# Optimization experiments

Measured on AMD Instinct MI355X. Metric: run time of the kernel, lower is better.

The kernel has to match this reference:

```python
import jax, jax.numpy as jnp
import numpy as np

D_X, D_Y, HIDDEN, K = 256, 32, 256, 2
T = 50
SIG_MIN, SIG_MAX = 0.002, 1.0
N = 4096
D_XY = D_X + D_Y
D_IN = D_XY + 2 * HIDDEN  # 800


def setup_inputs() -> dict:
    key = jax.random.key(0)
    ks = jax.random.split(key, 12)
    def w(k, shape, fan):
        return (jax.random.normal(k, shape, jnp.float32) / np.sqrt(fan)).astype(jnp.float32)
    return {
        "xy0": jax.random.normal(ks[0], (N, D_XY), jnp.float32) * SIG_MAX,  # randn * sigma_max * extra_noise(=1)
        "t0": jax.random.randint(ks[1], (N,), 0, K),
        "t_embed": w(ks[2], (K, HIDDEN), 1),
        "tm_w1": w(ks[3], (1, HIDDEN), 1), "tm_b1": jnp.zeros((HIDDEN,), jnp.float32),
        "tm_w2": w(ks[4], (HIDDEN, HIDDEN), HIDDEN), "tm_b2": jnp.zeros((HIDDEN,), jnp.float32),
        "tr_w1": w(ks[5], (D_IN, HIDDEN), D_IN), "tr_b1": jnp.zeros((HIDDEN,), jnp.float32),
        "tr_w2": w(ks[6], (HIDDEN, HIDDEN), HIDDEN), "tr_b2": jnp.zeros((HIDDEN,), jnp.float32),
        "sh_w": w(ks[7], (HIDDEN, D_XY), HIDDEN), "sh_b": jnp.zeros((D_XY,), jnp.float32),
        "ch_w": w(ks[8], (HIDDEN, K), HIDDEN), "ch_b": jnp.zeros((K,), jnp.float32),
    }


def _sigma(t):
    return SIG_MIN * (SIG_MAX / SIG_MIN) ** t


def reference(xy0, t0, t_embed, tm_w1, tm_b1, tm_w2, tm_b2,
              tr_w1, tr_b1, tr_w2, tr_b2, sh_w, sh_b, ch_w, ch_b):
    n = xy0.shape[0]
    silu = jax.nn.silu
    base_key = jax.random.key(42)

    def net(xy, t, tau):
        te = t_embed[t]  # (n, H) embedding lookup
        # time_mlp on scalar tau -> (H,), broadcast over batch (tau is identical per row)
        tm = silu(tau * tm_w1[0] + tm_b1) @ tm_w2 + tm_b2
        tm = jnp.broadcast_to(tm, (n, HIDDEN))
        h = jnp.concatenate([xy, te, tm], axis=-1)  # (n, D_IN)
        h = silu(silu(h @ tr_w1 + tr_b1) @ tr_w2 + tr_b2)
        return h @ sh_w + sh_b, h @ ch_w + ch_b  # score (n, D_XY), logits (n, K)

    def body(carry, t_idx):
        xy, t = carry
        tau = t_idx.astype(jnp.float32) / T
        sig_t = _sigma(tau)
        sig_prev = _sigma((t_idx - 1).astype(jnp.float32) / T)
        step = sig_t ** 2 - sig_prev ** 2  # positive reverse-SDE step size
        score, logits = net(xy, t, tau)
        k1, k2 = jax.random.split(jax.random.fold_in(base_key, t_idx))
        xy = xy + step * score + jnp.sqrt(step) * jax.random.normal(k1, xy.shape, xy.dtype)
        t = jax.random.categorical(k2, logits, axis=-1)  # multinomial(softmax(logits), 1)
        return (xy, t), None

    steps = jnp.arange(T - 1, 0, -1)  # reversed(range(1, T))
    (xy, t), _ = jax.lax.scan(body, (xy0, t0), steps)
    return xy[:, :D_X], xy[:, D_X:], t
```

## Files before the change

### kernel.cpp

```cpp
#include <hip/hip_runtime.h>
#include <math.h>


#define DXY 288
#define HID 256
#define NTHR 512
#define XYP 292
#define HP  260
#define OUT_Y_OFF 1048576
#define OUT_T_OFF 1179648
#define STEP_OFF 25600
#define WS_SWE 25728

typedef unsigned int u32;

__device__ __forceinline__ void tf2x32(u32 k0, u32 k1, u32 x0, u32 x1, u32& o0, u32& o1) {
  u32 ks2 = k0 ^ k1 ^ 0x1BD11BDAu;
#define TFR(r) { x0 += x1; x1 = (x1 << (r)) | (x1 >> (32 - (r))); x1 ^= x0; }
  x0 += k0; x1 += k1;
  TFR(13) TFR(15) TFR(26) TFR(6)
  x0 += k1;  x1 += ks2 + 1u;
  TFR(17) TFR(29) TFR(16) TFR(24)
  x0 += ks2; x1 += k0 + 2u;
  TFR(13) TFR(15) TFR(26) TFR(6)
  x0 += k0;  x1 += k1 + 3u;
  TFR(17) TFR(29) TFR(16) TFR(24)
  x0 += k1;  x1 += ks2 + 4u;
  TFR(13) TFR(15) TFR(26) TFR(6)
  x0 += ks2; x1 += k0 + 5u;
#undef TFR
  o0 = x0; o1 = x1;
}

__device__ __forceinline__ u32 pbits(u32 ka, u32 kb, u32 j) {
  u32 w0, w1;
  tf2x32(ka, kb, 0u, j, w0, w1);
  return w0 ^ w1;
}

__device__ __forceinline__ float u01f(u32 bits) {
  union { u32 i; float f; } v;
  v.i = (bits >> 9) | 0x3F800000u;
  return v.f - 1.0f;
}

__device__ __forceinline__ float erfinv32(float x) {
  float w = -log1pf(-x * x);
  float p;
  if (w < 5.0f) {
    w -= 2.5f;
    p = 2.81022636e-08f;
    p = fmaf(p, w, 3.43273939e-07f);
    p = fmaf(p, w, -3.5233877e-06f);
    p = fmaf(p, w, -4.39150654e-06f);
    p = fmaf(p, w, 0.00021858087f);
    p = fmaf(p, w, -0.00125372503f);
    p = fmaf(p, w, -0.00417768164f);
    p = fmaf(p, w, 0.246640727f);
    p = fmaf(p, w, 1.50140941f);
  } else {
    w = sqrtf(w) - 3.0f;
    p = -0.000200214257f;
    p = fmaf(p, w, 0.000100950558f);
    p = fmaf(p, w, 0.00134934322f);
    p = fmaf(p, w, -0.00367342844f);
    p = fmaf(p, w, 0.00573950773f);
    p = fmaf(p, w, -0.0076224613f);
    p = fmaf(p, w, 0.00943887047f);
    p = fmaf(p, w, 1.00167406f);
    p = fmaf(p, w, 2.83297682f);
  }
  return p * x;
}

__device__ __forceinline__ float nrmf(u32 bits) {
  float val = fmaf(u01f(bits), 2.0f, -0.99999994f);
  return 1.41421356f * erfinv32(val);
}
__device__ __forceinline__ float gumf(u32 bits) {
  float u = fmaxf(u01f(bits), 1.17549435e-38f);
  return -logf(-logf(u));
}
__device__ __forceinline__ float siluf(float x) {
  return x / (1.0f + expf(-x));
}

struct B8 { float4 a0, a1, a2, a3, b0, b1, b2, b3; };

__device__ __forceinline__ void fma8x4(float acc[4], const float4 x0, const float4 x1, const B8& B) {
  acc[0]=fmaf(x0.x,B.a0.x,acc[0]); acc[1]=fmaf(x0.x,B.a0.y,acc[1]); acc[2]=fmaf(x0.x,B.a0.z,acc[2]); acc[3]=fmaf(x0.x,B.a0.w,acc[3]);
  acc[0]=fmaf(x0.y,B.a1.x,acc[0]); acc[1]=fmaf(x0.y,B.a1.y,acc[1]); acc[2]=fmaf(x0.y,B.a1.z,acc[2]); acc[3]=fmaf(x0.y,B.a1.w,acc[3]);
  acc[0]=fmaf(x0.z,B.a2.x,acc[0]); acc[1]=fmaf(x0.z,B.a2.y,acc[1]); acc[2]=fmaf(x0.z,B.a2.z,acc[2]); acc[3]=fmaf(x0.z,B.a2.w,acc[3]);
  acc[0]=fmaf(x0.w,B.a3.x,acc[0]); acc[1]=fmaf(x0.w,B.a3.y,acc[1]); acc[2]=fmaf(x0.w,B.a3.z,acc[2]); acc[3]=fmaf(x0.w,B.a3.w,acc[3]);
  acc[0]=fmaf(x1.x,B.b0.x,acc[0]); acc[1]=fmaf(x1.x,B.b0.y,acc[1]); acc[2]=fmaf(x1.x,B.b0.z,acc[2]); acc[3]=fmaf(x1.x,B.b0.w,acc[3]);
  acc[0]=fmaf(x1.y,B.b1.x,acc[0]); acc[1]=fmaf(x1.y,B.b1.y,acc[1]); acc[2]=fmaf(x1.y,B.b1.z,acc[2]); acc[3]=fmaf(x1.y,B.b1.w,acc[3]);
  acc[0]=fmaf(x1.z,B.b2.x,acc[0]); acc[1]=fmaf(x1.z,B.b2.y,acc[1]); acc[2]=fmaf(x1.z,B.b2.z,acc[2]); acc[3]=fmaf(x1.z,B.b2.w,acc[3]);
  acc[0]=fmaf(x1.w,B.b3.x,acc[0]); acc[1]=fmaf(x1.w,B.b3.y,acc[1]); acc[2]=fmaf(x1.w,B.b3.z,acc[2]); acc[3]=fmaf(x1.w,B.b3.w,acc[3]);
}

__device__ __forceinline__ void gll16(const float* g, float* l) {
  __builtin_amdgcn_global_load_lds((const __attribute__((address_space(1))) void*)g,
                                   (__attribute__((address_space(3))) void*)l, 16, 0, 0);
}

__device__ __forceinline__ void issue_stage(int seq, float* buf, int tid,
                                            const float* w1, const float* w2,
                                            const float* sw) {
  if (seq < 17) {
    const float* src = (seq < 9) ? (w1 + seq * 8192) : (w2 + (seq - 9) * 8192);
    #pragma unroll
    for (int j = 0; j < 4; ++j) {
      int u = j * 512 + tid;
      gll16(src + u * 4, buf + u * 4);
    }
  } else {
    const int t0 = (seq - 17) * 32;
    #pragma unroll
    for (int j = 0; j < 4; ++j) {
      int u = j * 512 + tid;
      int r = u >> 6, c4 = (u & 63) << 2;
      gll16(sw + (t0 + r) * DXY + c4, buf + u * 4);
    }
  }
}

__device__ __forceinline__ void tile_mm(float accA[4], float accB[4],
                                        const float* tile, const float* aA,
                                        const float* aB, int cg) {
  #pragma unroll
  for (int kk = 0; kk < 32; kk += 8) {
    const float* tp = tile + kk * 256 + cg;
    B8 B;
    B.a0 = *(const float4*)(tp);
    B.a1 = *(const float4*)(tp + 256);
    B.a2 = *(const float4*)(tp + 512);
    B.a3 = *(const float4*)(tp + 768);
    B.b0 = *(const float4*)(tp + 1024);
    B.b1 = *(const float4*)(tp + 1280);
    B.b2 = *(const float4*)(tp + 1536);
    B.b3 = *(const float4*)(tp + 1792);
    float4 xA0 = *(const float4*)(aA + kk), xA1 = *(const float4*)(aA + kk + 4);
    float4 xB0 = *(const float4*)(aB + kk), xB1 = *(const float4*)(aB + kk + 4);
    fma8x4(accA, xA0, xA1, B);
    fma8x4(accB, xB0, xB1, B);
  }
}

__device__ __forceinline__ void tile_sync() {
  asm volatile("s_waitcnt vmcnt(4)" ::: "memory");
  asm volatile("s_waitcnt lgkmcnt(0)" ::: "memory");
  __builtin_amdgcn_s_barrier();
  __builtin_amdgcn_sched_barrier(0);
}

__global__ void precompute_ct(
    const float* __restrict__ t_embed,
    const float* __restrict__ tm_w1, const float* __restrict__ tm_b1,
    const float* __restrict__ tm_w2, const float* __restrict__ tm_b2,
    const float* __restrict__ tr_w1, const float* __restrict__ tr_b1,
    float* __restrict__ ws)
{
  const int t = blockIdx.x + 1;
  const int c = threadIdx.x;
  __shared__ float tmpre[HID];
  __shared__ float tmv[HID];
  const float tau = (float)t / 50.0f;

  tmpre[c] = siluf(fmaf(tau, tm_w1[c], tm_b1[c]));
  __syncthreads();
  {
    float acc = tm_b2[c];
    for (int i = 0; i < HID; i++)
      acc = fmaf(tmpre[i], tm_w2[i * HID + c], acc);
    tmv[c] = acc;
  }
  __syncthreads();
  float D = 0.f;
  for (int i = 0; i < HID; i++)
    D = fmaf(tmv[i], tr_w1[(544 + i) * HID + c], D);
  float ce0 = tr_b1[c], ce1 = tr_b1[c];
  for (int i = 0; i < HID; i++) {
    ce0 = fmaf(t_embed[i], tr_w1[(288 + i) * HID + c], ce0);
    ce1 = fmaf(t_embed[HID + i], tr_w1[(288 + i) * HID + c], ce1);
  }
  ws[t * 512 + c] = ce0 + D;
  ws[t * 512 + 256 + c] = ce1 + D;

  if (c == 0) {
    const double lt = 6.214608098422191;
    float sig_t = (float)(0.002 * exp(((double)t / 50.0) * lt));
    float sig_p = (float)(0.002 * exp(((double)(t - 1) / 50.0) * lt));
    float stepf = sig_t * sig_t - sig_p * sig_p;
    ws[STEP_OFF + 2 * t] = stepf;
    ws[STEP_OFF + 2 * t + 1] = sqrtf(stepf);
  }
}

__global__ void transpose_swe(const float* __restrict__ sw, float* __restrict__ ws)
{
  int i = blockIdx.x * 256 + threadIdx.x;
  int c = i >> 8, k = i & 255;
  ws[WS_SWE + c * 256 + k] = sw[k * DXY + 256 + c];
}

__global__ __launch_bounds__(NTHR, 2) void sampler_k(
    const float* __restrict__ xy0, const int* __restrict__ t0,
    const float* __restrict__ tr_w1,
    const float* __restrict__ tr_w2, const float* __restrict__ tr_b2,
    const float* __restrict__ sh_w, const float* __restrict__ sh_b,
    const float* __restrict__ ch_w, const float* __restrict__ ch_b,
    const float* __restrict__ ws,
    float* __restrict__ out)
{
  __shared__ float wt[3][8192];
  __shared__ float xy_s[16][XYP];
  __shared__ float h1_s[16][HP];
  __shared__ float h2_s[16][HP];
  __shared__ int tcur_s[16];

  const int tid = threadIdx.x;
  const int lane = tid & 63;
  const int w = tid >> 6;
  const int row0g = blockIdx.x * 16;

  const int r0 = lane >> 3;
  const int r1 = r0 + 8;
  const int cg = w * 32 + (lane & 7) * 4;
  const int rE = lane >> 2;
  const int cEl = w * 4 + (lane & 3);

  issue_stage(0, wt[0], tid, tr_w1, tr_w2, sh_w);
  issue_stage(1, wt[1], tid, tr_w1, tr_w2, sh_w);

  for (int idx = tid; idx < 16 * (DXY / 4); idx += NTHR) {
    int r = idx / (DXY / 4);
    int q = idx - r * (DXY / 4);
    *(float4*)&xy_s[r][q * 4] = *(const float4*)(xy0 + (row0g + r) * DXY + q * 4);
  }
  if (tid < 16) tcur_s[tid] = t0[row0g + tid];

  float chw0[4], chw1[4];
  #pragma unroll
  for (int j = 0; j < 4; j++) {
    chw0[j] = ch_w[(lane * 4 + j) * 2 + 0];
    chw1[j] = ch_w[(lane * 4 + j) * 2 + 1];
  }
  const float4 b2r = *(const float4*)(tr_b2 + cg);
  const float cb0 = ch_b[0], cb1 = ch_b[1];
  const float4 sbm = *(const float4*)(sh_b + cg);
  const float sbE = sh_b[256 + cEl];
  const float* epb = ws + WS_SWE + cEl * 256;
  __syncthreads();

  int q = 0;
  int cur = 0;
  int gb = 2;

  #pragma unroll 1
  for (int t_idx = 49; t_idx >= 1; --t_idx) {
    const float stepf = ws[STEP_OFF + 2 * t_idx];
    const float sstep = ws[STEP_OFF + 2 * t_idx + 1];

    u32 f0, f1, k1a, k1b, k2a, k2b;
    tf2x32(0u, 42u, 0u, (u32)t_idx, f0, f1);
    tf2x32(f0, f1, 0u, 0u, k1a, k1b);
    tf2x32(f0, f1, 0u, 1u, k2a, k2b);

    const int tc0 = tcur_s[r0], tc1 = tcur_s[r1];
    const float* ctp = ws + t_idx * 512;
    const float4 ctA = *(const float4*)(ctp + tc0 * 256 + cg);
    const float4 ctB = *(const float4*)(ctp + tc1 * 256 + cg);

    {
      float accA[4] = {0.f, 0.f, 0.f, 0.f};
      float accB[4] = {0.f, 0.f, 0.f, 0.f};
      #pragma unroll 1
      for (int s = 0; s < 9; ++s) {
        tile_sync();
        int nx = q + 2; if (nx >= 25) nx -= 25;
        issue_stage(nx, wt[gb], tid, tr_w1, tr_w2, sh_w);
        tile_mm(accA, accB, wt[cur], &xy_s[r0][s * 32], &xy_s[r1][s * 32], cg);
        q = (q + 1 == 25) ? 0 : q + 1;
        cur = (cur + 1 == 3) ? 0 : cur + 1;
        gb = (gb + 1 == 3) ? 0 : gb + 1;
      }
      float4 oA, oB;
      oA.x = siluf(accA[0] + ctA.x); oA.y = siluf(accA[1] + ctA.y);
      oA.z = siluf(accA[2] + ctA.z); oA.w = siluf(accA[3] + ctA.w);
      oB.x = siluf(accB[0] + ctB.x); oB.y = siluf(accB[1] + ctB.y);
      oB.z = siluf(accB[2] + ctB.z); oB.w = siluf(accB[3] + ctB.w);
      *(float4*)&h1_s[r0][cg] = oA;
      *(float4*)&h1_s[r1][cg] = oB;
    }

    {
      float accA[4] = {0.f, 0.f, 0.f, 0.f};
      float accB[4] = {0.f, 0.f, 0.f, 0.f};
      #pragma unroll 1
      for (int s = 0; s < 8; ++s) {
        tile_sync();
        int nx = q + 2; if (nx >= 25) nx -= 25;
        issue_stage(nx, wt[gb], tid, tr_w1, tr_w2, sh_w);
        tile_mm(accA, accB, wt[cur], &h1_s[r0][s * 32], &h1_s[r1][s * 32], cg);
        q = (q + 1 == 25) ? 0 : q + 1;
        cur = (cur + 1 == 3) ? 0 : cur + 1;
        gb = (gb + 1 == 3) ? 0 : gb + 1;
      }
      float4 oA, oB;
      oA.x = siluf(accA[0] + b2r.x); oA.y = siluf(accA[1] + b2r.y);
      oA.z = siluf(accA[2] + b2r.z); oA.w = siluf(accA[3] + b2r.w);
      oB.x = siluf(accB[0] + b2r.x); oB.y = siluf(accB[1] + b2r.y);
      oB.z = siluf(accB[2] + b2r.z); oB.w = siluf(accB[3] + b2r.w);
      *(float4*)&h2_s[r0][cg] = oA;
      *(float4*)&h2_s[r1][cg] = oB;
    }

    {
      float accA[4] = {0.f, 0.f, 0.f, 0.f};
      float accB[4] = {0.f, 0.f, 0.f, 0.f};
      #pragma unroll 1
      for (int s = 0; s < 8; ++s) {
        tile_sync();
        int nx = q + 2; if (nx >= 25) nx -= 25;
        issue_stage(nx, wt[gb], tid, tr_w1, tr_w2, sh_w);
        if (s == 0) {
          float4 hL0 = *(const float4*)&h2_s[2 * w][lane * 4];
          float4 hL1 = *(const float4*)&h2_s[2 * w + 1][lane * 4];
          float pA0 = hL0.x * chw0[0] + hL0.y * chw0[1] + hL0.z * chw0[2] + hL0.w * chw0[3];
          float pA1 = hL0.x * chw1[0] + hL0.y * chw1[1] + hL0.z * chw1[2] + hL0.w * chw1[3];
          float pB0 = hL1.x * chw0[0] + hL1.y * chw0[1] + hL1.z * chw0[2] + hL1.w * chw0[3];
          float pB1 = hL1.x * chw1[0] + hL1.y * chw1[1] + hL1.z * chw1[2] + hL1.w * chw1[3];
          #pragma unroll
          for (int off = 32; off > 0; off >>= 1) {
            pA0 += __shfl_xor(pA0, off);
            pA1 += __shfl_xor(pA1, off);
            pB0 += __shfl_xor(pB0, off);
            pB1 += __shfl_xor(pB1, off);
          }
          u32 grow = (u32)(row0g + 2 * w + ((lane >> 1) & 1));
          float g = gumf(pbits(k2a, k2b, grow * 2u + (u32)(lane & 1)));
          float g0 = __shfl(g, 0), g1 = __shfl(g, 1);
          float g2 = __shfl(g, 2), g3 = __shfl(g, 3);
          if (lane == 0) {
            tcur_s[2 * w]     = (pA1 + cb1 + g1 > pA0 + cb0 + g0) ? 1 : 0;
            tcur_s[2 * w + 1] = (pB1 + cb1 + g3 > pB0 + cb0 + g2) ? 1 : 0;
          }
        }
        tile_mm(accA, accB, wt[cur], &h2_s[r0][s * 32], &h2_s[r1][s * 32], cg);
        q = (q + 1 == 25) ? 0 : q + 1;
        cur = (cur + 1 == 3) ? 0 : cur + 1;
        gb = (gb + 1 == 3) ? 0 : gb + 1;
      }
      const u32 jA = (u32)(row0g + r0) * 288u + (u32)cg;
      const u32 jB = (u32)(row0g + r1) * 288u + (u32)cg;
      float4 xA = *(const float4*)&xy_s[r0][cg];
      float4 xB = *(const float4*)&xy_s[r1][cg];
      xA.x = fmaf(sstep, nrmf(pbits(k1a, k1b, jA + 0u)), fmaf(stepf, accA[0] + sbm.x, xA.x));
      xA.y = fmaf(sstep, nrmf(pbits(k1a, k1b, jA + 1u)), fmaf(stepf, accA[1] + sbm.y, xA.y));
      xA.z = fmaf(sstep, nrmf(pbits(k1a, k1b, jA + 2u)), fmaf(stepf, accA[2] + sbm.z, xA.z));
      xA.w = fmaf(sstep, nrmf(pbits(k1a, k1b, jA + 3u)), fmaf(stepf, accA[3] + sbm.w, xA.w));
      xB.x = fmaf(sstep, nrmf(pbits(k1a, k1b, jB + 0u)), fmaf(stepf, accB[0] + sbm.x, xB.x));
      xB.y = fmaf(sstep, nrmf(pbits(k1a, k1b, jB + 1u)), fmaf(stepf, accB[1] + sbm.y, xB.y));
      xB.z = fmaf(sstep, nrmf(pbits(k1a, k1b, jB + 2u)), fmaf(stepf, accB[2] + sbm.z, xB.z));
      xB.w = fmaf(sstep, nrmf(pbits(k1a, k1b, jB + 3u)), fmaf(stepf, accB[3] + sbm.w, xB.w));
      *(float4*)&xy_s[r0][cg] = xA;
      *(float4*)&xy_s[r1][cg] = xB;

      float sE0 = 0.f, sE1 = 0.f;
      #pragma unroll 4
      for (int k = 0; k < 256; k += 8) {
        float4 h0  = *(const float4*)&h2_s[rE][k];
        float4 h1v = *(const float4*)&h2_s[rE][k + 4];
        float4 wa = *(const float4*)(epb + k);
        float4 wb = *(const float4*)(epb + k + 4);
        sE0 = fmaf(h0.w, wa.w, fmaf(h0.z, wa.z, fmaf(h0.y, wa.y, fmaf(h0.x, wa.x, sE0))));
        sE1 = fmaf(h1v.w, wb.w, fmaf(h1v.z, wb.z, fmaf(h1v.y, wb.y, fmaf(h1v.x, wb.x, sE1))));
      }
      float sE = sE0 + sE1;
      u32 jE = (u32)(row0g + rE) * 288u + (u32)(256 + cEl);
      float nE = nrmf(pbits(k1a, k1b, jE));
      xy_s[rE][256 + cEl] = fmaf(sstep, nE, fmaf(stepf, sE + sbE, xy_s[rE][256 + cEl]));
    }
  }

  __syncthreads();

  for (int idx = tid; idx < 16 * 64; idx += NTHR) {
    int r = idx >> 6;
    int c4 = (idx & 63) * 4;
    *(float4*)(out + (row0g + r) * 256 + c4) = *(const float4*)&xy_s[r][c4];
  }
  for (int idx = tid; idx < 16 * 8; idx += NTHR) {
    int r = idx >> 3;
    int c4 = (idx & 7) * 4;
    *(float4*)(out + OUT_Y_OFF + (row0g + r) * 32 + c4) = *(const float4*)&xy_s[r][256 + c4];
  }
  if (tid < 16) out[OUT_T_OFF + row0g + tid] = (float)tcur_s[tid];
}

extern "C" void kernel_launch(void* const* d_in, const int* in_sizes, int n_in,
                              void* d_out, int out_size, void* d_ws, size_t ws_size,
                              hipStream_t stream) {
  (void)in_sizes; (void)n_in; (void)ws_size; (void)out_size;
  const float* xy0     = (const float*)d_in[0];
  const int*   t0      = (const int*)d_in[1];
  const float* t_embed = (const float*)d_in[2];
  const float* tm_w1   = (const float*)d_in[3];
  const float* tm_b1   = (const float*)d_in[4];
  const float* tm_w2   = (const float*)d_in[5];
  const float* tm_b2   = (const float*)d_in[6];
  const float* tr_w1   = (const float*)d_in[7];
  const float* tr_b1   = (const float*)d_in[8];
  const float* tr_w2   = (const float*)d_in[9];
  const float* tr_b2   = (const float*)d_in[10];
  const float* sh_w    = (const float*)d_in[11];
  const float* sh_b    = (const float*)d_in[12];
  const float* ch_w    = (const float*)d_in[13];
  const float* ch_b    = (const float*)d_in[14];
  float* ws  = (float*)d_ws;
  float* out = (float*)d_out;

  precompute_ct<<<49, 256, 0, stream>>>(t_embed, tm_w1, tm_b1, tm_w2, tm_b2,
                                        tr_w1, tr_b1, ws);
  transpose_swe<<<32, 256, 0, stream>>>(sh_w, ws);
  sampler_k<<<256, NTHR, 0, stream>>>(xy0, t0, tr_w1, tr_w2, tr_b2,
                                      sh_w, sh_b, ch_w, ch_b, ws, out);
}
```

Baseline: 2.556 ms.

## Split warps: two stream weights via LDS, six read weights directly from global

The LDS weight staging buffer shrinks from 3x8192 to 3x2048 floats. Only the first two waves (columns 0-63) now use the async global-to-LDS pipeline. The other six waves read their weight columns straight from global/L2 with register double-buffering, in lockstep through plain barriers. This cuts LDS footprint and LDS traffic, which may allow more occupancy, but it relies on L2/cache bandwidth for most weight reads. The barrier counts of the two paths must match, and the logits sampling is moved out of the score loop behind its own barrier.

```diff
diff --git a/kernel.cpp b/kernel.cpp
--- a/kernel.cpp
+++ b/kernel.cpp
@@ -98,29 +98,38 @@
   acc[0]=fmaf(x1.w,B.b3.x,acc[0]); acc[1]=fmaf(x1.w,B.b3.y,acc[1]); acc[2]=fmaf(x1.w,B.b3.z,acc[2]); acc[3]=fmaf(x1.w,B.b3.w,acc[3]);
 }
 
+template<int LD>
+__device__ __forceinline__ void loadB8(B8& B, const float* p, int kk) {
+  const float* q = p + kk * LD;
+  const float* q2 = q + 4 * LD;
+  B.a0 = *(const float4*)(q);
+  B.a1 = *(const float4*)(q + LD);
+  B.a2 = *(const float4*)(q + 2 * LD);
+  B.a3 = *(const float4*)(q + 3 * LD);
+  B.b0 = *(const float4*)(q2);
+  B.b1 = *(const float4*)(q2 + LD);
+  B.b2 = *(const float4*)(q2 + 2 * LD);
+  B.b3 = *(const float4*)(q2 + 3 * LD);
+}
+
 __device__ __forceinline__ void gll16(const float* g, float* l) {
   __builtin_amdgcn_global_load_lds((const __attribute__((address_space(1))) void*)g,
                                    (__attribute__((address_space(3))) void*)l, 16, 0, 0);
 }
 
-__device__ __forceinline__ void issue_stage(int seq, float* buf, int tid,
+__device__ __forceinline__ void issue_stage(int seq, float* buf, int t128,
                                             const float* w1, const float* w2,
                                             const float* sw) {
-  if (seq < 17) {
-    const float* src = (seq < 9) ? (w1 + seq * 8192) : (w2 + (seq - 9) * 8192);
-    #pragma unroll
-    for (int j = 0; j < 4; ++j) {
-      int u = j * 512 + tid;
-      gll16(src + u * 4, buf + u * 4);
-    }
-  } else {
-    const int t0 = (seq - 17) * 32;
-    #pragma unroll
-    for (int j = 0; j < 4; ++j) {
-      int u = j * 512 + tid;
-      int r = u >> 6, c4 = (u & 63) << 2;
-      gll16(sw + (t0 + r) * DXY + c4, buf + u * 4);
-    }
+  const float* src;
+  int ld;
+  if (seq < 9)       { src = w1 + seq * 8192;        ld = 256; }
+  else if (seq < 17) { src = w2 + (seq - 9) * 8192;  ld = 256; }
+  else               { src = sw + (seq - 17) * 9216; ld = 288; }
+  #pragma unroll
+  for (int j = 0; j < 4; ++j) {
+    int u = j * 128 + t128;
+    int r = u >> 4, c4 = (u & 15) << 2;
+    gll16(src + r * ld + c4, buf + u * 4);
   }
 }
 
@@ -129,16 +138,16 @@
                                         const float* aB, int cg) {
   #pragma unroll
   for (int kk = 0; kk < 32; kk += 8) {
-    const float* tp = tile + kk * 256 + cg;
+    const float* tp = tile + kk * 64 + cg;
     B8 B;
     B.a0 = *(const float4*)(tp);
-    B.a1 = *(const float4*)(tp + 256);
-    B.a2 = *(const float4*)(tp + 512);
-    B.a3 = *(const float4*)(tp + 768);
-    B.b0 = *(const float4*)(tp + 1024);
-    B.b1 = *(const float4*)(tp + 1280);
-    B.b2 = *(const float4*)(tp + 1536);
-    B.b3 = *(const float4*)(tp + 1792);
+    B.a1 = *(const float4*)(tp + 64);
+    B.a2 = *(const float4*)(tp + 128);
+    B.a3 = *(const float4*)(tp + 192);
+    B.b0 = *(const float4*)(tp + 256);
+    B.b1 = *(const float4*)(tp + 320);
+    B.b2 = *(const float4*)(tp + 384);
+    B.b3 = *(const float4*)(tp + 448);
     float4 xA0 = *(const float4*)(aA + kk), xA1 = *(const float4*)(aA + kk + 4);
     float4 xB0 = *(const float4*)(aB + kk), xB1 = *(const float4*)(aB + kk + 4);
     fma8x4(accA, xA0, xA1, B);
@@ -146,11 +155,50 @@
   }
 }
 
-__device__ __forceinline__ void tile_sync() {
+__device__ __forceinline__ void sync_l() {
   asm volatile("s_waitcnt vmcnt(4)" ::: "memory");
   asm volatile("s_waitcnt lgkmcnt(0)" ::: "memory");
   __builtin_amdgcn_s_barrier();
   __builtin_amdgcn_sched_barrier(0);
+}
+__device__ __forceinline__ void sync_g() {
+  asm volatile("s_waitcnt lgkmcnt(0)" ::: "memory");
+  __builtin_amdgcn_s_barrier();
+  __builtin_amdgcn_sched_barrier(0);
+}
+
+template<int LD, int K>
+__device__ __forceinline__ void phase_global(float accA[4], float accB[4],
+                                             const float* wp, const float* aA,
+                                             const float* aB) {
+  B8 Bp, Bq;
+  float4 xA0, xA1, xB0, xB1;
+  loadB8<LD>(Bp, wp, 0);
+  #pragma unroll 1
+  for (int s = 0; s < K / 32; ++s) {
+    sync_g();
+    if (s == 0) {
+      xA0 = *(const float4*)(aA);     xA1 = *(const float4*)(aA + 4);
+      xB0 = *(const float4*)(aB);     xB1 = *(const float4*)(aB + 4);
+    }
+    #pragma unroll
+    for (int h = 0; h < 2; ++h) {
+      const int j = s * 2 + h;
+      const int k1 = j * 16 + 8;
+      const int k2t = j * 16 + 16;
+      const int k2 = (k2t < K) ? k2t : 0;
+      loadB8<LD>(Bq, wp, k1);
+      float4 yA0 = *(const float4*)(aA + k1), yA1 = *(const float4*)(aA + k1 + 4);
+      float4 yB0 = *(const float4*)(aB + k1), yB1 = *(const float4*)(aB + k1 + 4);
+      fma8x4(accA, xA0, xA1, Bp);
+      fma8x4(accB, xB0, xB1, Bp);
+      loadB8<LD>(Bp, wp, k2);
+      xA0 = *(const float4*)(aA + k2); xA1 = *(const float4*)(aA + k2 + 4);
+      xB0 = *(const float4*)(aB + k2); xB1 = *(const float4*)(aB + k2 + 4);
+      fma8x4(accA, yA0, yA1, Bq);
+      fma8x4(accB, yB0, yB1, Bq);
+    }
+  }
 }
 
 __global__ void precompute_ct(
@@ -212,7 +260,7 @@
     const float* __restrict__ ws,
     float* __restrict__ out)
 {
-  __shared__ float wt[3][8192];
+  __shared__ float wt[3][2048];
   __shared__ float xy_s[16][XYP];
   __shared__ float h1_s[16][HP];
   __shared__ float h2_s[16][HP];
@@ -225,17 +273,20 @@
 
   const int r0 = lane >> 3;
   const int r1 = r0 + 8;
-  const int cg = w * 32 + (lane & 7) * 4;
+  const bool isL = (w < 2);
+  const int cg = isL ? (w * 32 + (lane & 7) * 4)
+                     : (64 + (w - 2) * 32 + (lane & 7) * 4);
   const int rE = lane >> 2;
   const int cEl = w * 4 + (lane & 3);
 
-  issue_stage(0, wt[0], tid, tr_w1, tr_w2, sh_w);
-  issue_stage(1, wt[1], tid, tr_w1, tr_w2, sh_w);
-
+  if (isL) {
+    issue_stage(0, wt[0], tid, tr_w1, tr_w2, sh_w);
+    issue_stage(1, wt[1], tid, tr_w1, tr_w2, sh_w);
+  }
   for (int idx = tid; idx < 16 * (DXY / 4); idx += NTHR) {
     int r = idx / (DXY / 4);
-    int q = idx - r * (DXY / 4);
-    *(float4*)&xy_s[r][q * 4] = *(const float4*)(xy0 + (row0g + r) * DXY + q * 4);
+    int q2 = idx - r * (DXY / 4);
+    *(float4*)&xy_s[r][q2 * 4] = *(const float4*)(xy0 + (row0g + r) * DXY + q2 * 4);
   }
   if (tid < 16) tcur_s[tid] = t0[row0g + tid];
 
@@ -252,9 +303,7 @@
   const float* epb = ws + WS_SWE + cEl * 256;
   __syncthreads();
 
-  int q = 0;
-  int cur = 0;
-  int gb = 2;
+  int q = 0, cur = 0, gb = 2;
 
   #pragma unroll 1
   for (int t_idx = 49; t_idx >= 1; --t_idx) {
@@ -274,15 +323,19 @@
     {
       float accA[4] = {0.f, 0.f, 0.f, 0.f};
       float accB[4] = {0.f, 0.f, 0.f, 0.f};
-      #pragma unroll 1
-      for (int s = 0; s < 9; ++s) {
-        tile_sync();
-        int nx = q + 2; if (nx >= 25) nx -= 25;
-        issue_stage(nx, wt[gb], tid, tr_w1, tr_w2, sh_w);
-        tile_mm(accA, accB, wt[cur], &xy_s[r0][s * 32], &xy_s[r1][s * 32], cg);
-        q = (q + 1 == 25) ? 0 : q + 1;
-        cur = (cur + 1 == 3) ? 0 : cur + 1;
-        gb = (gb + 1 == 3) ? 0 : gb + 1;
+      if (isL) {
+        #pragma unroll 1
+        for (int s = 0; s < 9; ++s) {
+          sync_l();
+          int nx = q + 2; if (nx >= 25) nx -= 25;
+          issue_stage(nx, wt[gb], tid, tr_w1, tr_w2, sh_w);
+          tile_mm(accA, accB, wt[cur], &xy_s[r0][s * 32], &xy_s[r1][s * 32], cg);
+          q = (q + 1 == 25) ? 0 : q + 1;
+          cur = (cur + 1 == 3) ? 0 : cur + 1;
+          gb = (gb + 1 == 3) ? 0 : gb + 1;
+        }
+      } else {
+        phase_global<HID, 288>(accA, accB, tr_w1 + cg, &xy_s[r0][0], &xy_s[r1][0]);
       }
       float4 oA, oB;
       oA.x = siluf(accA[0] + ctA.x); oA.y = siluf(accA[1] + ctA.y);
@@ -296,15 +349,19 @@
     {
       float accA[4] = {0.f, 0.f, 0.f, 0.f};
       float accB[4] = {0.f, 0.f, 0.f, 0.f};
-      #pragma unroll 1
-      for (int s = 0; s < 8; ++s) {
-        tile_sync();
-        int nx = q + 2; if (nx >= 25) nx -= 25;
-        issue_stage(nx, wt[gb], tid, tr_w1, tr_w2, sh_w);
-        tile_mm(accA, accB, wt[cur], &h1_s[r0][s * 32], &h1_s[r1][s * 32], cg);
-        q = (q + 1 == 25) ? 0 : q + 1;
-        cur = (cur + 1 == 3) ? 0 : cur + 1;
-        gb = (gb + 1 == 3) ? 0 : gb + 1;
+      if (isL) {
+        #pragma unroll 1
+        for (int s = 0; s < 8; ++s) {
+          sync_l();
+          int nx = q + 2; if (nx >= 25) nx -= 25;
+          issue_stage(nx, wt[gb], tid, tr_w1, tr_w2, sh_w);
+          tile_mm(accA, accB, wt[cur], &h1_s[r0][s * 32], &h1_s[r1][s * 32], cg);
+          q = (q + 1 == 25) ? 0 : q + 1;
+          cur = (cur + 1 == 3) ? 0 : cur + 1;
+          gb = (gb + 1 == 3) ? 0 : gb + 1;
+        }
+      } else {
+        phase_global<HID, 256>(accA, accB, tr_w2 + cg, &h1_s[r0][0], &h1_s[r1][0]);
       }
       float4 oA, oB;
       oA.x = siluf(accA[0] + b2r.x); oA.y = siluf(accA[1] + b2r.y);
@@ -315,41 +372,47 @@
       *(float4*)&h2_s[r1][cg] = oB;
     }
 
+    sync_g();
+    {
+      float4 hL0 = *(const float4*)&h2_s[2 * w][lane * 4];
+      float4 hL1 = *(const float4*)&h2_s[2 * w + 1][lane * 4];
+      float pA0 = hL0.x * chw0[0] + hL0.y * chw0[1] + hL0.z * chw0[2] + hL0.w * chw0[3];
+      float pA1 = hL0.x * chw1[0] + hL0.y * chw1[1] + hL0.z * chw1[2] + hL0.w * chw1[3];
+      float pB0 = hL1.x * chw0[0] + hL1.y * chw0[1] + hL1.z * chw0[2] + hL1.w * chw0[3];
+      float pB1 = hL1.x * chw1[0] + hL1.y * chw1[1] + hL1.z * chw1[2] + hL1.w * chw1[3];
+      #pragma unroll
+      for (int off = 32; off > 0; off >>= 1) {
+        pA0 += __shfl_xor(pA0, off);
+        pA1 += __shfl_xor(pA1, off);
+        pB0 += __shfl_xor(pB0, off);
+        pB1 += __shfl_xor(pB1, off);
+      }
+      u32 grow = (u32)(row0g + 2 * w + ((lane >> 1) & 1));
+      float g = gumf(pbits(k2a, k2b, grow * 2u + (u32)(lane & 1)));
+      float g0 = __shfl(g, 0), g1 = __shfl(g, 1);
+      float g2 = __shfl(g, 2), g3 = __shfl(g, 3);
+      if (lane == 0) {
+        tcur_s[2 * w]     = (pA1 + cb1 + g1 > pA0 + cb0 + g0) ? 1 : 0;
+        tcur_s[2 * w + 1] = (pB1 + cb1 + g3 > pB0 + cb0 + g2) ? 1 : 0;
+      }
+    }
+
     {
       float accA[4] = {0.f, 0.f, 0.f, 0.f};
       float accB[4] = {0.f, 0.f, 0.f, 0.f};
-      #pragma unroll 1
-      for (int s = 0; s < 8; ++s) {
-        tile_sync();
-        int nx = q + 2; if (nx >= 25) nx -= 25;
-        issue_stage(nx, wt[gb], tid, tr_w1, tr_w2, sh_w);
-        if (s == 0) {
-          float4 hL0 = *(const float4*)&h2_s[2 * w][lane * 4];
-          float4 hL1 = *(const float4*)&h2_s[2 * w + 1][lane * 4];
-          float pA0 = hL0.x * chw0[0] + hL0.y * chw0[1] + hL0.z * chw0[2] + hL0.w * chw0[3];
-          float pA1 = hL0.x * chw1[0] + hL0.y * chw1[1] + hL0.z * chw1[2] + hL0.w * chw1[3];
-          float pB0 = hL1.x * chw0[0] + hL1.y * chw0[1] + hL1.z * chw0[2] + hL1.w * chw0[3];
-          float pB1 = hL1.x * chw1[0] + hL1.y * chw1[1] + hL1.z * chw1[2] + hL1.w * chw1[3];
-          #pragma unroll
-          for (int off = 32; off > 0; off >>= 1) {
-            pA0 += __shfl_xor(pA0, off);
-            pA1 += __shfl_xor(pA1, off);
-            pB0 += __shfl_xor(pB0, off);
-            pB1 += __shfl_xor(pB1, off);
-          }
-          u32 grow = (u32)(row0g + 2 * w + ((lane >> 1) & 1));
-          float g = gumf(pbits(k2a, k2b, grow * 2u + (u32)(lane & 1)));
-          float g0 = __shfl(g, 0), g1 = __shfl(g, 1);
-          float g2 = __shfl(g, 2), g3 = __shfl(g, 3);
-          if (lane == 0) {
-            tcur_s[2 * w]     = (pA1 + cb1 + g1 > pA0 + cb0 + g0) ? 1 : 0;
-            tcur_s[2 * w + 1] = (pB1 + cb1 + g3 > pB0 + cb0 + g2) ? 1 : 0;
-          }
+      if (isL) {
+        #pragma unroll 1
+        for (int s = 0; s < 8; ++s) {
+          sync_l();
+          int nx = q + 2; if (nx >= 25) nx -= 25;
+          issue_stage(nx, wt[gb], tid, tr_w1, tr_w2, sh_w);
+          tile_mm(accA, accB, wt[cur], &h2_s[r0][s * 32], &h2_s[r1][s * 32], cg);
+          q = (q + 1 == 25) ? 0 : q + 1;
+          cur = (cur + 1 == 3) ? 0 : cur + 1;
+          gb = (gb + 1 == 3) ? 0 : gb + 1;
         }
-        tile_mm(accA, accB, wt[cur], &h2_s[r0][s * 32], &h2_s[r1][s * 32], cg);
-        q = (q + 1 == 25) ? 0 : q + 1;
-        cur = (cur + 1 == 3) ? 0 : cur + 1;
-        gb = (gb + 1 == 3) ? 0 : gb + 1;
+      } else {
+        phase_global<DXY, 256>(accA, accB, sh_w + cg, &h2_s[r0][0], &h2_s[r1][0]);
       }
       const u32 jA = (u32)(row0g + r0) * 288u + (u32)cg;
       const u32 jB = (u32)(row0g + r1) * 288u + (u32)cg;
```

Result: slower. 3.051 ms (+19.3%).
